# Kernel tuning notes

Measured on AMD Instinct MI355X. Metric: run time of the kernel, lower is better.

Reference implementation:

```python
import math
import jax, jax.numpy as jnp
import numpy as np

B, T, D = 4, 2048, 1024
H = 16
DK = D // H


def setup_inputs() -> dict:
    key = jax.random.key(0)
    ks = jax.random.split(key, 9)
    s = 1.0 / math.sqrt(D)
    return {
        "x": jax.random.normal(ks[0], (B, T, D), dtype=jnp.float32),
        "Wq": jax.random.normal(ks[1], (D, D), dtype=jnp.float32) * s,
        "bq": jax.random.normal(ks[2], (D,), dtype=jnp.float32) * s,
        "Wk": jax.random.normal(ks[3], (D, D), dtype=jnp.float32) * s,
        "bk": jax.random.normal(ks[4], (D,), dtype=jnp.float32) * s,
        "Wv": jax.random.normal(ks[5], (D, D), dtype=jnp.float32) * s,
        "bv": jax.random.normal(ks[6], (D,), dtype=jnp.float32) * s,
        "Wo": jax.random.normal(ks[7], (D, D), dtype=jnp.float32) * s,
        "bo": jax.random.normal(ks[8], (D,), dtype=jnp.float32) * s,
    }


def reference(x, Wq, bq, Wk, bk, Wv, bv, Wo, bo):
    Bx, Tx, C = x.shape
    # projections -> [B, H, T, d_k]
    q = (x @ Wq + bq).reshape(Bx, Tx, H, DK).transpose(0, 2, 1, 3)
    k = (x @ Wk + bk).reshape(Bx, Tx, H, DK).transpose(0, 2, 1, 3)
    v = (x @ Wv + bv).reshape(Bx, Tx, H, DK).transpose(0, 2, 1, 3)
    # scores [B, H, T, T], scaled
    scores = jnp.einsum("bhqd,bhkd->bhqk", q, k) / math.sqrt(DK)
    causal = jnp.tril(jnp.ones((Tx, Tx), dtype=bool))
    scores = jnp.where(causal[None, None, :, :], scores, -jnp.inf)
    attn = jax.nn.softmax(scores, axis=-1)  # dropout p=0.0 (eval)
    out = jnp.einsum("bhqk,bhkd->bhqd", attn, v)
    out = out.transpose(0, 2, 1, 3).reshape(Bx, Tx, C)
    return out @ Wo + bo
```

## Files before the change

kernel.cpp:

```cpp
#include <hip/hip_runtime.h>
#include <stdint.h>
#include <math.h>

typedef __attribute__((ext_vector_type(8))) __bf16 bf16x8;
typedef __attribute__((ext_vector_type(4))) __bf16 bf16x4;
typedef __attribute__((ext_vector_type(4))) float f32x4;

__device__ __forceinline__ void load_lds16(const void* g, void* l) {
  __builtin_amdgcn_global_load_lds((__attribute__((address_space(1))) void*)(g),
                                   (__attribute__((address_space(3))) void*)(l),
                                   16, 0, 0);
}

__device__ __forceinline__ uint32_t pack_bf2(float a, float b) {
  union { __bf16 h; uint16_t u; } x, y;
  x.h = (__bf16)a; y.h = (__bf16)b;
  return (uint32_t)x.u | ((uint32_t)y.u << 16);
}

__global__ __launch_bounds__(256)
void convert_x(const float* __restrict__ xf, __bf16* __restrict__ xb) {
  const size_t i = ((size_t)blockIdx.x * 256 + threadIdx.x) * 8;
  const float4 u0 = *(const float4*)(xf + i);
  const float4 u1 = *(const float4*)(xf + i + 4);
  bf16x8 v;
  v[0] = (__bf16)u0.x; v[1] = (__bf16)u0.y; v[2] = (__bf16)u0.z; v[3] = (__bf16)u0.w;
  v[4] = (__bf16)u1.x; v[5] = (__bf16)u1.y; v[6] = (__bf16)u1.z; v[7] = (__bf16)u1.w;
  *(bf16x8*)&xb[i] = v;
}

__global__ __launch_bounds__(256)
void prep_weights(const float* __restrict__ Wq, const float* __restrict__ Wk,
                  const float* __restrict__ Wv, const float* __restrict__ Wo,
                  const float* __restrict__ bq, const float* __restrict__ bk,
                  const float* __restrict__ bv, const float* __restrict__ bo,
                  __bf16* __restrict__ Bt1, __bf16* __restrict__ Bt2,
                  float* __restrict__ bqkv, float* __restrict__ bo_f) {
  const int m = blockIdx.z;
  const float* W = (m == 0) ? Wq : (m == 1) ? Wk : (m == 2) ? Wv : Wo;
  __bf16* Out = (m == 3) ? Bt2 : Bt1 + (size_t)m * 1024 * 1024;
  const int kt = blockIdx.x * 64, nt = blockIdx.y * 64;
  __shared__ __bf16 tile[64 * 68];
  const int t = threadIdx.x;
#pragma unroll
  for (int i = 0; i < 16; i++) {
    int e = i * 256 + t;
    int r = e >> 6, c = e & 63;
    tile[r * 68 + c] = (__bf16)W[(size_t)(kt + r) * 1024 + nt + c];
  }
  __syncthreads();
#pragma unroll
  for (int i = 0; i < 16; i++) {
    int e = i * 256 + t;
    int r = e >> 6, c = e & 63;
    Out[(size_t)(nt + r) * 1024 + kt + c] = tile[c * 68 + r];
  }
  if (blockIdx.x == 0 && blockIdx.y == 0) {
    if (m < 3) {
      const float* bsrc = (m == 0) ? bq : (m == 1) ? bk : bv;
      for (int i = t; i < 1024; i += 256) bqkv[m * 1024 + i] = bsrc[i];
    } else {
      for (int i = t; i < 1024; i += 256) bo_f[i] = bo[i];
    }
  }
}

__global__ __launch_bounds__(256)
void gemm_bt(const __bf16* __restrict__ A, const __bf16* __restrict__ Bt,
             const float* __restrict__ bias, void* __restrict__ Cv,
             int out_f32, int M, int N, int K) {
  __shared__ __align__(16) __bf16 As[128 * 32];
  __shared__ __align__(16) __bf16 Bs[128 * 32];
  const int t = threadIdx.x;
  const int lane = t & 63;
  const int wave = t >> 6;
  const int bm = blockIdx.x * 128;
  const int bn = blockIdx.y * 128;
  const int wm = (wave >> 1) * 64;
  const int wn = (wave & 1) * 64;
  const int fm = lane & 15, fk = (lane >> 4) * 8;
  f32x4 acc[4][4] = {};

  const int r0 = t >> 2, kc = (t & 3) * 8;
  const __bf16* Ag0 = A + (size_t)(bm + r0) * K + kc;
  const __bf16* Ag1 = A + (size_t)(bm + 64 + r0) * K + kc;
  const __bf16* Bg0 = Bt + (size_t)(bn + r0) * K + kc;
  const __bf16* Bg1 = Bt + (size_t)(bn + 64 + r0) * K + kc;

  for (int k0 = 0; k0 < K; k0 += 32) {
    load_lds16(Ag0 + k0, &As[t * 8]);
    load_lds16(Ag1 + k0, &As[2048 + t * 8]);
    load_lds16(Bg0 + k0, &Bs[t * 8]);
    load_lds16(Bg1 + k0, &Bs[2048 + t * 8]);
    asm volatile("s_waitcnt vmcnt(0)" ::: "memory");
    __syncthreads();
    bf16x8 af[4], bfr[4];
#pragma unroll
    for (int i = 0; i < 4; i++) {
      af[i] = *(const bf16x8*)&As[(wm + i * 16 + fm) * 32 + fk];
      bfr[i] = *(const bf16x8*)&Bs[(wn + i * 16 + fm) * 32 + fk];
    }
#pragma unroll
    for (int i = 0; i < 4; i++)
#pragma unroll
      for (int j = 0; j < 4; j++)
        acc[i][j] = __builtin_amdgcn_mfma_f32_16x16x32_bf16(af[i], bfr[j], acc[i][j], 0, 0, 0);
    __syncthreads();
  }

  const int cm = (lane >> 4) * 4, cn = lane & 15;
#pragma unroll
  for (int i = 0; i < 4; i++)
#pragma unroll
    for (int j = 0; j < 4; j++) {
      const int col = bn + wn + j * 16 + cn;
      const float bvv = bias[col];
#pragma unroll
      for (int r = 0; r < 4; r++) {
        const int row = bm + wm + i * 16 + cm + r;
        const float val = acc[i][j][r] + bvv;
        if (out_f32) ((float*)Cv)[(size_t)row * N + col] = val;
        else ((__bf16*)Cv)[(size_t)row * N + col] = (__bf16)val;
      }
    }
}

__global__ __launch_bounds__(256)
void transpose_v(const __bf16* __restrict__ QKV, __bf16* __restrict__ Vt) {
  const int tt = blockIdx.x;
  const int bh = blockIdx.y;
  const int b = bh >> 4, h = bh & 15;
  __shared__ __bf16 tile[64 * 68];
  const int t = threadIdx.x;
#pragma unroll
  for (int i = 0; i < 16; i++) {
    int e = i * 256 + t;
    int tok = e >> 6, dk = e & 63;
    tile[tok * 68 + dk] =
        QKV[((size_t)b * 2048 + tt * 64 + tok) * 3072 + 2048 + h * 64 + dk];
  }
  __syncthreads();
#pragma unroll
  for (int i = 0; i < 16; i++) {
    int e = i * 256 + t;
    int dk = e >> 6, tok = e & 63;
    Vt[((size_t)bh * 64 + dk) * 2048 + tt * 64 + tok] = tile[tok * 68 + dk];
  }
}

__global__ __launch_bounds__(256)
void flash_attn(const __bf16* __restrict__ QKV, const __bf16* __restrict__ Vt,
                __bf16* __restrict__ O) {
  const int y = blockIdx.y;
  const int g = y >> 2, iy = y & 3;
  const int qt = (g == 0) ? (15 - 2 * iy)
               : (g == 1) ? (2 * iy)
               : (g == 2) ? (14 - 2 * iy)
                          : (2 * iy + 1);
  const int bh = blockIdx.x;
  const int b = bh >> 4, h = bh & 15;
  __shared__ __align__(16) __bf16 Ks[2][64 * 64];
  __shared__ __align__(16) __bf16 Vs[2][64 * 64];
  const int t = threadIdx.x, lane = t & 63, wave = t >> 6;
  const int fm = lane & 15, fq = lane >> 4;
  const int tok0 = t >> 3;
  const int csw = ((t & 7) ^ (tok0 & 7)) << 3;
  const int swb = (fm & 7) << 4;
  const int rb0 = (((fq << 4)) ^ swb) >> 1;
  const int rb1 = ((64 + (fq << 4)) ^ swb) >> 1;

  const size_t kbase = ((size_t)b * 2048) * 3072 + 1024 + h * 64;
  const size_t vbase = (size_t)bh * 64 * 2048;
  const int nkt = 2 * qt + 2;
  const int qw = qt * 128 + wave * 32;
  const int qmax_w = qw + 31;
  const float SC = 0.18033688011112042f;

  bf16x8 qf[2][2];
#pragma unroll
  for (int mi = 0; mi < 2; mi++) {
    const size_t qrow = ((size_t)b * 2048 + qw + mi * 16 + fm) * 3072 + h * 64;
    qf[mi][0] = *(const bf16x8*)&QKV[qrow + fq * 8];
    qf[mi][1] = *(const bf16x8*)&QKV[qrow + 32 + fq * 8];
  }

  f32x4 o_acc[2][4] = {};
  float m_i[2] = {-1e30f, -1e30f}, l_i[2] = {0.f, 0.f};

  const int srcA = ((lane & 16) << 1) | fm;
  const int srcB = srcA + 16;
  const bool sel_hi = (lane & 32) != 0;

#define STAGE(KT, BUF)                                                          \
  {                                                                             \
    const int kb2 = (KT) * 64;                                                  \
    load_lds16(&QKV[kbase + (size_t)(kb2 + tok0) * 3072 + csw],                 \
               &Ks[BUF][t * 8]);                                                \
    load_lds16(&QKV[kbase + (size_t)(kb2 + 32 + tok0) * 3072 + csw],            \
               &Ks[BUF][2048 + t * 8]);                                         \
    load_lds16(&Vt[vbase + (size_t)tok0 * 2048 + kb2 + csw],                    \
               &Vs[BUF][t * 8]);                                                \
    load_lds16(&Vt[vbase + (size_t)(tok0 + 32) * 2048 + kb2 + csw],             \
               &Vs[BUF][2048 + t * 8]);                                         \
  }

  STAGE(0, 0);
  __syncthreads();
  int cur = 0;

  for (int kt = 0; kt < nkt; kt++) {
    const int kb = kt * 64;
    if (kt + 1 < nkt) STAGE(kt + 1, cur ^ 1);

    if (kb <= qmax_w) {
      const __bf16* Kc = Ks[cur];
      const __bf16* Vc = Vs[cur];

      f32x4 s[2][4];
      __builtin_amdgcn_s_setprio(1);
#pragma unroll
      for (int nt = 0; nt < 4; nt++) {
        const bf16x8 kf0 = *(const bf16x8*)&Kc[(nt * 16 + fm) * 64 + rb0];
        const bf16x8 kf1 = *(const bf16x8*)&Kc[(nt * 16 + fm) * 64 + rb1];
#pragma unroll
        for (int mi = 0; mi < 2; mi++) {
          f32x4 z = {};
          z = __builtin_amdgcn_mfma_f32_16x16x32_bf16(kf0, qf[mi][0], z, 0, 0, 0);
          z = __builtin_amdgcn_mfma_f32_16x16x32_bf16(kf1, qf[mi][1], z, 0, 0, 0);
          s[mi][nt] = z;
        }
      }
      __builtin_amdgcn_s_setprio(0);

      if (kb + 63 > qw) {
#pragma unroll
        for (int mi = 0; mi < 2; mi++) {
          const int qq = qw + mi * 16 + fm;
#pragma unroll
          for (int nt = 0; nt < 4; nt++) {
            const int kk = kb + nt * 16 + fq * 4;
#pragma unroll
            for (int r = 0; r < 4; r++) {
              float v = s[mi][nt][r] * SC;
              if (kk + r > qq) v = -1e30f;
              s[mi][nt][r] = v;
            }
          }
        }
      } else {
#pragma unroll
        for (int mi = 0; mi < 2; mi++)
#pragma unroll
          for (int nt = 0; nt < 4; nt++)
#pragma unroll
            for (int r = 0; r < 4; r++) s[mi][nt][r] *= SC;
      }

      float rmax[2];
#pragma unroll
      for (int mi = 0; mi < 2; mi++) {
        float a = fmaxf(fmaxf(s[mi][0][0], s[mi][0][1]),
                        fmaxf(s[mi][0][2], s[mi][0][3]));
#pragma unroll
        for (int nt = 1; nt < 4; nt++)
          a = fmaxf(a, fmaxf(fmaxf(s[mi][nt][0], s[mi][nt][1]),
                             fmaxf(s[mi][nt][2], s[mi][nt][3])));
        a = fmaxf(a, __shfl_xor(a, 16, 64));
        a = fmaxf(a, __shfl_xor(a, 32, 64));
        rmax[mi] = a;
      }

      const float grow = fmaxf(rmax[0] - m_i[0], rmax[1] - m_i[1]);
      if (!__all(grow <= 8.0f)) {
#pragma unroll
        for (int mi = 0; mi < 2; mi++) {
          const float mn = fmaxf(m_i[mi], rmax[mi]);
          const float a = exp2f(m_i[mi] - mn);
          m_i[mi] = mn;
          l_i[mi] *= a;
#pragma unroll
          for (int dt = 0; dt < 4; dt++)
#pragma unroll
            for (int r = 0; r < 4; r++) o_acc[mi][dt][r] *= a;
        }
      }

#pragma unroll
      for (int mi = 0; mi < 2; mi++) {
        float sum = 0.f;
#pragma unroll
        for (int nt = 0; nt < 4; nt++)
#pragma unroll
          for (int r = 0; r < 4; r++) {
            const float p = exp2f(s[mi][nt][r] - m_i[mi]);
            s[mi][nt][r] = p;
            sum += p;
          }
        sum += __shfl_xor(sum, 16, 64);
        sum += __shfl_xor(sum, 32, 64);
        l_i[mi] += sum;
      }

      uint32_t u[2][4][2];
#pragma unroll
      for (int mi = 0; mi < 2; mi++)
#pragma unroll
        for (int nt = 0; nt < 4; nt++) {
          u[mi][nt][0] = pack_bf2(s[mi][nt][0], s[mi][nt][1]);
          u[mi][nt][1] = pack_bf2(s[mi][nt][2], s[mi][nt][3]);
        }

      union U8 { bf16x8 v; uint32_t d[4]; };
      U8 pb[2][2];
#pragma unroll
      for (int mi = 0; mi < 2; mi++)
#pragma unroll
        for (int c = 0; c < 2; c++) {
          const uint32_t a0 = __shfl((int)u[mi][2 * c][0], srcA, 64);
          const uint32_t b0 = __shfl((int)u[mi][2 * c + 1][0], srcA, 64);
          const uint32_t a1 = __shfl((int)u[mi][2 * c][1], srcA, 64);
          const uint32_t b1 = __shfl((int)u[mi][2 * c + 1][1], srcA, 64);
          const uint32_t a2 = __shfl((int)u[mi][2 * c][0], srcB, 64);
          const uint32_t b2 = __shfl((int)u[mi][2 * c + 1][0], srcB, 64);
          const uint32_t a3 = __shfl((int)u[mi][2 * c][1], srcB, 64);
          const uint32_t b3 = __shfl((int)u[mi][2 * c + 1][1], srcB, 64);
          pb[mi][c].d[0] = sel_hi ? b0 : a0;
          pb[mi][c].d[1] = sel_hi ? b1 : a1;
          pb[mi][c].d[2] = sel_hi ? b2 : a2;
          pb[mi][c].d[3] = sel_hi ? b3 : a3;
        }

      __builtin_amdgcn_s_setprio(1);
#pragma unroll
      for (int dt = 0; dt < 4; dt++) {
        const bf16x8 vf0 = *(const bf16x8*)&Vc[(dt * 16 + fm) * 64 + rb0];
        const bf16x8 vf1 = *(const bf16x8*)&Vc[(dt * 16 + fm) * 64 + rb1];
#pragma unroll
        for (int mi = 0; mi < 2; mi++) {
          f32x4 o = o_acc[mi][dt];
          o = __builtin_amdgcn_mfma_f32_16x16x32_bf16(vf0, pb[mi][0].v, o, 0, 0, 0);
          o = __builtin_amdgcn_mfma_f32_16x16x32_bf16(vf1, pb[mi][1].v, o, 0, 0, 0);
          o_acc[mi][dt] = o;
        }
      }
      __builtin_amdgcn_s_setprio(0);
    }

    __syncthreads();
    cur ^= 1;
  }

#pragma unroll
  for (int mi = 0; mi < 2; mi++) {
    const float linv = 1.f / l_i[mi];
    const size_t orow = (size_t)b * 2048 + qw + mi * 16 + fm;
#pragma unroll
    for (int dt = 0; dt < 4; dt++) {
      bf16x4 w;
#pragma unroll
      for (int r = 0; r < 4; r++) w[r] = (__bf16)(o_acc[mi][dt][r] * linv);
      *(bf16x4*)&O[orow * 1024 + h * 64 + dt * 16 + fq * 4] = w;
    }
  }
#undef STAGE
}

extern "C" void kernel_launch(void* const* d_in, const int* in_sizes, int n_in,
                              void* d_out, int out_size, void* d_ws, size_t ws_size,
                              hipStream_t stream) {
  const float* x = (const float*)d_in[0];
  const float* Wq = (const float*)d_in[1];
  const float* bq = (const float*)d_in[2];
  const float* Wk = (const float*)d_in[3];
  const float* bk = (const float*)d_in[4];
  const float* Wv = (const float*)d_in[5];
  const float* bv = (const float*)d_in[6];
  const float* Wo = (const float*)d_in[7];
  const float* bo = (const float*)d_in[8];

  char* ws = (char*)d_ws;
  __bf16* Bt1 = (__bf16*)(ws);
  __bf16* Bt2 = (__bf16*)(ws + 6291456);
  float* bqkv = (float*)(ws + 8388608);
  float* bo_f = (float*)(ws + 8400896);
  __bf16* QKV = (__bf16*)(ws + 8405504);
  __bf16* Vt = (__bf16*)(ws + 58737152);
  __bf16* Xb = (__bf16*)(ws + 75514368);
  __bf16* Ow = Xb;

  hipLaunchKernelGGL(convert_x, dim3(4096), dim3(256), 0, stream, x, Xb);
  hipLaunchKernelGGL(prep_weights, dim3(16, 16, 4), dim3(256), 0, stream,
                     Wq, Wk, Wv, Wo, bq, bk, bv, bo, Bt1, Bt2, bqkv, bo_f);
  hipLaunchKernelGGL(gemm_bt, dim3(64, 24), dim3(256), 0, stream,
                     Xb, Bt1, bqkv, (void*)QKV, 0, 8192, 3072, 1024);
  hipLaunchKernelGGL(transpose_v, dim3(32, 64), dim3(256), 0, stream, QKV, Vt);
  hipLaunchKernelGGL(flash_attn, dim3(64, 16), dim3(256), 0, stream, QKV, Vt, Ow);
  hipLaunchKernelGGL(gemm_bt, dim3(64, 8), dim3(256), 0, stream,
                     Ow, Bt2, bo_f, d_out, 1, 8192, 1024, 1024);
}
```

Baseline: 326.8 us.

## Use 16x16x16 MFMA for PV to skip P shuffles; row sums via MFMA

The PV product now uses the 16x16x16 bf16 MFMA, whose operand layout matches the score accumulator layout. This removes the cross-lane shuffle and select sequence that repacked P for the 16x16x32 instruction, at the cost of twice as many MFMA issues with narrower V reads from LDS. Row sums of P are computed by an MFMA against a vector of ones instead of shuffle reductions, and the softmax scale is folded into the exp2 argument with an fma. The causal query-tile ordering across blockIdx.y is also changed.

Result: no change. 329.1 us (+0.7%).

```diff
diff --git a/kernel.cpp b/kernel.cpp
--- a/kernel.cpp
+++ b/kernel.cpp
@@ -5,6 +5,7 @@
 typedef __attribute__((ext_vector_type(8))) __bf16 bf16x8;
 typedef __attribute__((ext_vector_type(4))) __bf16 bf16x4;
 typedef __attribute__((ext_vector_type(4))) float f32x4;
+typedef __attribute__((ext_vector_type(4))) short short4v;
 
 __device__ __forceinline__ void load_lds16(const void* g, void* l) {
   __builtin_amdgcn_global_load_lds((__attribute__((address_space(1))) void*)(g),
@@ -16,6 +17,22 @@
   union { __bf16 h; uint16_t u; } x, y;
   x.h = (__bf16)a; y.h = (__bf16)b;
   return (uint32_t)x.u | ((uint32_t)y.u << 16);
+}
+
+__device__ __forceinline__ short4v mk4(uint32_t lo, uint32_t hi) {
+  union { uint32_t d[2]; short4v v; } u;
+  u.d[0] = lo; u.d[1] = hi;
+  return u.v;
+}
+
+__device__ __forceinline__ f32x4 mfma16(short4v a, short4v b, f32x4 c) {
+#if defined(__has_builtin) && __has_builtin(__builtin_amdgcn_mfma_f32_16x16x16bf16_1k)
+  return __builtin_amdgcn_mfma_f32_16x16x16bf16_1k(a, b, c, 0, 0, 0);
+#else
+  asm volatile("v_mfma_f32_16x16x16_bf16 %0, %1, %2, %0"
+               : "+v"(c) : "v"(a), "v"(b));
+  return c;
+#endif
 }
 
 __global__ __launch_bounds__(256)
@@ -153,10 +170,10 @@
                 __bf16* __restrict__ O) {
   const int y = blockIdx.y;
   const int g = y >> 2, iy = y & 3;
-  const int qt = (g == 0) ? (15 - 2 * iy)
-               : (g == 1) ? (2 * iy)
-               : (g == 2) ? (14 - 2 * iy)
-                          : (2 * iy + 1);
+  const int qt = (g == 0) ? (15 - iy)
+               : (g == 1) ? iy
+               : (g == 2) ? (7 - iy)
+                          : (8 + iy);
   const int bh = blockIdx.x;
   const int b = bh >> 4, h = bh & 15;
   __shared__ __align__(16) __bf16 Ks[2][64 * 64];
@@ -168,6 +185,10 @@
   const int swb = (fm & 7) << 4;
   const int rb0 = (((fq << 4)) ^ swb) >> 1;
   const int rb1 = ((64 + (fq << 4)) ^ swb) >> 1;
+  int voff[4];
+#pragma unroll
+  for (int nt = 0; nt < 4; nt++)
+    voff[nt] = (((((nt << 1) | (fq >> 1))) ^ (fm & 7)) << 3) | ((fq & 1) << 2);
 
   const size_t kbase = ((size_t)b * 2048) * 3072 + 1024 + h * 64;
   const size_t vbase = (size_t)bh * 64 * 2048;
@@ -175,6 +196,7 @@
   const int qw = qt * 128 + wave * 32;
   const int qmax_w = qw + 31;
   const float SC = 0.18033688011112042f;
+  const float THR_RAW = 44.3614195558365f;
 
   bf16x8 qf[2][2];
 #pragma unroll
@@ -184,12 +206,10 @@
     qf[mi][1] = *(const bf16x8*)&QKV[qrow + 32 + fq * 8];
   }
 
+  const short4v ones4 = {(short)0x3F80, (short)0x3F80, (short)0x3F80, (short)0x3F80};
+
   f32x4 o_acc[2][4] = {};
   float m_i[2] = {-1e30f, -1e30f}, l_i[2] = {0.f, 0.f};
-
-  const int srcA = ((lane & 16) << 1) | fm;
-  const int srcB = srcA + 16;
-  const bool sel_hi = (lane & 32) != 0;
 
 #define STAGE(KT, BUF)                                                          \
   {                                                                             \
@@ -240,20 +260,10 @@
           for (int nt = 0; nt < 4; nt++) {
             const int kk = kb + nt * 16 + fq * 4;
 #pragma unroll
-            for (int r = 0; r < 4; r++) {
-              float v = s[mi][nt][r] * SC;
-              if (kk + r > qq) v = -1e30f;
-              s[mi][nt][r] = v;
-            }
+            for (int r = 0; r < 4; r++)
+              if (kk + r > qq) s[mi][nt][r] = -1e30f;
           }
         }
-      } else {
-#pragma unroll
-        for (int mi = 0; mi < 2; mi++)
-#pragma unroll
-          for (int nt = 0; nt < 4; nt++)
-#pragma unroll
-            for (int r = 0; r < 4; r++) s[mi][nt][r] *= SC;
       }
 
       float rmax[2];
@@ -271,11 +281,11 @@
       }
 
       const float grow = fmaxf(rmax[0] - m_i[0], rmax[1] - m_i[1]);
-      if (!__all(grow <= 8.0f)) {
+      if (!__all(grow <= THR_RAW)) {
 #pragma unroll
         for (int mi = 0; mi < 2; mi++) {
           const float mn = fmaxf(m_i[mi], rmax[mi]);
-          const float a = exp2f(m_i[mi] - mn);
+          const float a = exp2f(SC * (m_i[mi] - mn));
           m_i[mi] = mn;
           l_i[mi] *= a;
 #pragma unroll
@@ -285,65 +295,49 @@
         }
       }
 
+      short4v pb[2][4];
 #pragma unroll
       for (int mi = 0; mi < 2; mi++) {
-        float sum = 0.f;
+        const float msc = -SC * m_i[mi];
+#pragma unroll
+        for (int nt = 0; nt < 4; nt++) {
+          const float p0 = exp2f(fmaf(s[mi][nt][0], SC, msc));
+          const float p1 = exp2f(fmaf(s[mi][nt][1], SC, msc));
+          const float p2 = exp2f(fmaf(s[mi][nt][2], SC, msc));
+          const float p3 = exp2f(fmaf(s[mi][nt][3], SC, msc));
+          pb[mi][nt] = mk4(pack_bf2(p0, p1), pack_bf2(p2, p3));
+        }
+      }
+
+      f32x4 rsv[2];
+#pragma unroll
+      for (int mi = 0; mi < 2; mi++) {
+        f32x4 rs = {};
+#pragma unroll
+        for (int nt = 0; nt < 4; nt++) rs = mfma16(ones4, pb[mi][nt], rs);
+        rsv[mi] = rs;
+      }
+
+      __builtin_amdgcn_s_setprio(1);
+#pragma unroll
+      for (int dt = 0; dt < 4; dt++) {
+        const int rowb = (dt * 16 + fm) * 64;
+        short4v vf[4];
 #pragma unroll
         for (int nt = 0; nt < 4; nt++)
-#pragma unroll
-          for (int r = 0; r < 4; r++) {
-            const float p = exp2f(s[mi][nt][r] - m_i[mi]);
-            s[mi][nt][r] = p;
-            sum += p;
-          }
-        sum += __shfl_xor(sum, 16, 64);
-        sum += __shfl_xor(sum, 32, 64);
-        l_i[mi] += sum;
-      }
-
-      uint32_t u[2][4][2];
-#pragma unroll
-      for (int mi = 0; mi < 2; mi++)
-#pragma unroll
-        for (int nt = 0; nt < 4; nt++) {
-          u[mi][nt][0] = pack_bf2(s[mi][nt][0], s[mi][nt][1]);
-          u[mi][nt][1] = pack_bf2(s[mi][nt][2], s[mi][nt][3]);
-        }
-
-      union U8 { bf16x8 v; uint32_t d[4]; };
-      U8 pb[2][2];
-#pragma unroll
-      for (int mi = 0; mi < 2; mi++)
-#pragma unroll
-        for (int c = 0; c < 2; c++) {
-          const uint32_t a0 = __shfl((int)u[mi][2 * c][0], srcA, 64);
-          const uint32_t b0 = __shfl((int)u[mi][2 * c + 1][0], srcA, 64);
-          const uint32_t a1 = __shfl((int)u[mi][2 * c][1], srcA, 64);
-          const uint32_t b1 = __shfl((int)u[mi][2 * c + 1][1], srcA, 64);
-          const uint32_t a2 = __shfl((int)u[mi][2 * c][0], srcB, 64);
-          const uint32_t b2 = __shfl((int)u[mi][2 * c + 1][0], srcB, 64);
-          const uint32_t a3 = __shfl((int)u[mi][2 * c][1], srcB, 64);
-          const uint32_t b3 = __shfl((int)u[mi][2 * c + 1][1], srcB, 64);
-          pb[mi][c].d[0] = sel_hi ? b0 : a0;
-          pb[mi][c].d[1] = sel_hi ? b1 : a1;
-          pb[mi][c].d[2] = sel_hi ? b2 : a2;
-          pb[mi][c].d[3] = sel_hi ? b3 : a3;
-        }
-
-      __builtin_amdgcn_s_setprio(1);
-#pragma unroll
-      for (int dt = 0; dt < 4; dt++) {
-        const bf16x8 vf0 = *(const bf16x8*)&Vc[(dt * 16 + fm) * 64 + rb0];
-        const bf16x8 vf1 = *(const bf16x8*)&Vc[(dt * 16 + fm) * 64 + rb1];
+          vf[nt] = *(const short4v*)&Vc[rowb + voff[nt]];
 #pragma unroll
         for (int mi = 0; mi < 2; mi++) {
           f32x4 o = o_acc[mi][dt];
-          o = __builtin_amdgcn_mfma_f32_16x16x32_bf16(vf0, pb[mi][0].v, o, 0, 0, 0);
-          o = __builtin_amdgcn_mfma_f32_16x16x32_bf16(vf1, pb[mi][1].v, o, 0, 0, 0);
+#pragma unroll
+          for (int nt = 0; nt < 4; nt++) o = mfma16(vf[nt], pb[mi][nt], o);
           o_acc[mi][dt] = o;
         }
       }
       __builtin_amdgcn_s_setprio(0);
+
+#pragma unroll
+      for (int mi = 0; mi < 2; mi++) l_i[mi] += rsv[mi][0];
     }
 
     __syncthreads();
```
